# Kernel optimization log

Measured on AMD Instinct MI355X. Metric: run time of the kernel, lower is better.

Reference implementation:

```python
import jax, jax.numpy as jnp
import numpy as np

HEADS = 4
DIM_HEAD = 128


def setup_inputs() -> dict:
    key = jax.random.key(0)
    k1, k2, k3, k4 = jax.random.split(key, 4)
    B, C, H, W = 8, 256, 64, 64
    hidden = HEADS * DIM_HEAD  # 512
    x = jax.random.normal(k1, (B, C, H, W), dtype=jnp.float32)
    # 1x1 convs are just channel matmuls; store kernels as [out_ch, in_ch]
    w_qkv = jax.random.normal(k2, (3 * hidden, C), dtype=jnp.float32) * 0.05
    w_out = jax.random.normal(k3, (C, hidden), dtype=jnp.float32) * 0.05
    b_out = jax.random.normal(k4, (C,), dtype=jnp.float32) * 0.05
    return {"x": x, "w_qkv": w_qkv, "w_out": w_out, "b_out": b_out}


def reference(x, w_qkv, w_out, b_out):
    B, C, H, W = x.shape
    n = H * W
    # to_qkv: 1x1 conv without bias == channel matmul
    qkv = jnp.einsum('bchw,oc->bohw', x, w_qkv)  # [B, 3*heads*dim_head, H, W]
    qkv = qkv.reshape(B, 3, HEADS, DIM_HEAD, n)  # 'b (qkv heads c) h w -> b qkv heads c n'
    q, k, v = qkv[:, 0], qkv[:, 1], qkv[:, 2]    # each [B, heads, dim_head, n]
    k = jax.nn.softmax(k, axis=-1)               # softmax over spatial positions
    context = jnp.einsum('bhdn,bhen->bhde', k, v)   # [B, heads, d, e]
    out = jnp.einsum('bhde,bhdn->bhen', context, q)  # [B, heads, e, n]
    out = out.reshape(B, HEADS * DIM_HEAD, H, W)
    # to_out: 1x1 conv with bias
    return jnp.einsum('bchw,oc->bohw', out, w_out) + b_out[None, :, None, None]
```

## Files before the change

kernel.cpp:

```cpp
#include <hip/hip_runtime.h>
#include <stdint.h>


#define TILE 64
#define BK 16

using frag8 = __attribute__((ext_vector_type(8))) short;
using f32x4 = __attribute__((ext_vector_type(4))) float;

__device__ __forceinline__ float bf2f(unsigned short u) {
    union { unsigned int u; float f; } c;
    c.u = ((unsigned int)u) << 16;
    return c.f;
}
__device__ __forceinline__ unsigned short f2bf(float f) {
    union { float f; unsigned int u; } c; c.f = f;
    unsigned int u = c.u;
    return (unsigned short)((u + 0x7FFFu + ((u >> 16) & 1u)) >> 16);
}

__device__ __forceinline__ void gl_lds16(const void* g, void* l) {
    __builtin_amdgcn_global_load_lds(
        (const __attribute__((address_space(1))) unsigned int*)g,
        (__attribute__((address_space(3))) unsigned int*)l, 16, 0, 0);
}

__global__ __launch_bounds__(256) void k0_wconv(
    const float* __restrict__ w_qkv, unsigned short* __restrict__ wkvb)
{
    const int idx = (blockIdx.x * 256 + threadIdx.x) * 4;
    float4 v = *(const float4*)(w_qkv + 512 * 256 + idx);
    ushort4 o;
    o.x = f2bf(v.x); o.y = f2bf(v.y); o.z = f2bf(v.z); o.w = f2bf(v.w);
    *(ushort4*)(wkvb + idx) = o;
}

__global__ __launch_bounds__(256) void k0_xt(
    const float* __restrict__ x, unsigned short* __restrict__ xbT)
{
    __shared__ float T[64][65];
    const int tid = threadIdx.x;
    const int n0 = blockIdx.x * 64, c0 = blockIdx.y * 64, b = blockIdx.z;
    const float* xb = x + (size_t)b * 1048576;
    const int cr = tid >> 4, nc = (tid & 15) * 4;
    #pragma unroll
    for (int p = 0; p < 4; ++p) {
        float4 v = *(const float4*)(xb + (size_t)(c0 + cr + p * 16) * 4096 + n0 + nc);
        T[cr + p * 16][nc + 0] = v.x; T[cr + p * 16][nc + 1] = v.y;
        T[cr + p * 16][nc + 2] = v.z; T[cr + p * 16][nc + 3] = v.w;
    }
    __syncthreads();
    const int n = tid >> 2, cc = (tid & 3) * 16;
    unsigned short* dst = xbT + (size_t)b * 1048576 + (size_t)(n0 + n) * 256 + c0 + cc;
    #pragma unroll
    for (int g = 0; g < 4; ++g) {
        ushort4 o;
        o.x = f2bf(T[cc + g * 4 + 0][n]);
        o.y = f2bf(T[cc + g * 4 + 1][n]);
        o.z = f2bf(T[cc + g * 4 + 2][n]);
        o.w = f2bf(T[cc + g * 4 + 3][n]);
        *(ushort4*)(dst + g * 4) = o;
    }
}

template<int MODE>
__global__ __launch_bounds__(256) void mfma_bt(
    const unsigned short* __restrict__ A0, int lda,
    const unsigned short* __restrict__ B0, int ldb,
    void* __restrict__ C0, int ldc,
    const float* __restrict__ bias, int Kp,
    unsigned long long sAz, unsigned long long sBz, unsigned long long sCz)
{
    __shared__ unsigned short As[128 * 32];
    __shared__ unsigned short Bs[128 * 32];
    const int tid  = threadIdx.x;
    const int w    = tid >> 6, lane = tid & 63;
    const int quad = lane >> 4, l16 = lane & 15;
    const int wm = (w >> 1) * 64, wn = (w & 1) * 64;
    const int z = blockIdx.z;

    const unsigned short* A;
    const unsigned short* B;
    int ks, ke, m0, n0;
    if constexpr (MODE == 2) {
        m0 = 0; n0 = 0;
        ks = blockIdx.x * 512; ke = ks + 512;
        const unsigned long long off =
            ((unsigned long long)(z >> 2) * 1024ull + (unsigned long long)(z & 3) * 128ull) * 4096ull;
        A = A0 + off; B = B0 + off;
    } else {
        m0 = blockIdx.y * 128; n0 = blockIdx.x * 128;
        ks = 0; ke = Kp;
        A = A0 + sAz * z + (unsigned long long)m0 * lda;
        B = B0 + sBz * z + (unsigned long long)n0 * ldb;
    }

    const int cA0 = w * 128 + lane;
    const int cA1 = cA0 + 64;
    const unsigned short* gA0 = A + (unsigned long long)(cA0 >> 2) * lda + (cA0 & 3) * 8;
    const unsigned short* gA1 = A + (unsigned long long)(cA1 >> 2) * lda + (cA1 & 3) * 8;
    const unsigned short* gB0 = B + (unsigned long long)(cA0 >> 2) * ldb + (cA0 & 3) * 8;
    const unsigned short* gB1 = B + (unsigned long long)(cA1 >> 2) * ldb + (cA1 & 3) * 8;
    unsigned short* lA0 = As + w * 1024;
    unsigned short* lA1 = As + w * 1024 + 512;
    unsigned short* lB0 = Bs + w * 1024;
    unsigned short* lB1 = Bs + w * 1024 + 512;

    f32x4 acc[4][4] = {};

    for (int k0 = ks; k0 < ke; k0 += 32) {
        gl_lds16(gA0 + k0, lA0);
        gl_lds16(gA1 + k0, lA1);
        gl_lds16(gB0 + k0, lB0);
        gl_lds16(gB1 + k0, lB1);
        __syncthreads();
        frag8 a[4], b[4];
        #pragma unroll
        for (int t = 0; t < 4; ++t) {
            a[t] = *(const frag8*)(As + (wm + t * 16 + l16) * 32 + quad * 8);
            b[t] = *(const frag8*)(Bs + (wn + t * 16 + l16) * 32 + quad * 8);
        }
        #pragma unroll
        for (int mt = 0; mt < 4; ++mt)
            #pragma unroll
            for (int nt = 0; nt < 4; ++nt)
                acc[mt][nt] = __builtin_amdgcn_mfma_f32_16x16x32_bf16(
                    a[mt], b[nt], acc[mt][nt], 0, 0, 0);
        __syncthreads();
    }

    if constexpr (MODE == 0) {
        unsigned short* C = (unsigned short*)C0 + sCz * z
                          + (unsigned long long)m0 * ldc + n0;
        #pragma unroll
        for (int mt = 0; mt < 4; ++mt) {
            const int row = wm + mt * 16 + quad * 4;
            #pragma unroll
            for (int nt = 0; nt < 4; ++nt) {
                const int col = wn + nt * 16 + l16;
                #pragma unroll
                for (int r = 0; r < 4; ++r)
                    C[(unsigned long long)(row + r) * ldc + col] = f2bf(acc[mt][nt][r]);
            }
        }
    } else if constexpr (MODE == 1) {
        float* C = (float*)C0 + sCz * z + (unsigned long long)m0 * ldc + n0;
        const float* bp = bias + m0;
        #pragma unroll
        for (int mt = 0; mt < 4; ++mt) {
            const int row = wm + mt * 16 + quad * 4;
            #pragma unroll
            for (int nt = 0; nt < 4; ++nt) {
                const int col = wn + nt * 16 + l16;
                #pragma unroll
                for (int r = 0; r < 4; ++r)
                    C[(unsigned long long)(row + r) * ldc + col] = acc[mt][nt][r] + bp[row + r];
            }
        }
    } else {
        float* C = (float*)C0 + ((unsigned long long)blockIdx.x * 32 + z) * 16384ull;
        #pragma unroll
        for (int mt = 0; mt < 4; ++mt) {
            const int row = wm + mt * 16 + quad * 4;
            #pragma unroll
            for (int nt = 0; nt < 4; ++nt) {
                const int col = wn + nt * 16 + l16;
                #pragma unroll
                for (int r = 0; r < 4; ++r)
                    C[(row + r) * 128 + col] = acc[mt][nt][r];
            }
        }
    }
}

__global__ __launch_bounds__(256) void k2_softmax(unsigned short* __restrict__ kv)
{
    __shared__ float red[4];
    const int idx = blockIdx.x;
    const int b = idx >> 9, r = idx & 511;
    unsigned short* row = kv + (size_t)(b * 1024 + r) * 4096;
    const int tid = threadIdx.x;
    float v[16];
    #pragma unroll
    for (int g = 0; g < 4; ++g) {
        ushort4 u = *(const ushort4*)(row + g * 1024 + tid * 4);
        v[g * 4 + 0] = bf2f(u.x); v[g * 4 + 1] = bf2f(u.y);
        v[g * 4 + 2] = bf2f(u.z); v[g * 4 + 3] = bf2f(u.w);
    }
    float m = -1e30f;
    #pragma unroll
    for (int i = 0; i < 16; ++i) m = fmaxf(m, v[i]);
    #pragma unroll
    for (int off = 32; off > 0; off >>= 1) m = fmaxf(m, __shfl_down(m, off, 64));
    if ((tid & 63) == 0) red[tid >> 6] = m;
    __syncthreads();
    m = fmaxf(fmaxf(red[0], red[1]), fmaxf(red[2], red[3]));
    __syncthreads();
    float s = 0.f;
    #pragma unroll
    for (int i = 0; i < 16; ++i) { v[i] = __expf(v[i] - m); s += v[i]; }
    #pragma unroll
    for (int off = 32; off > 0; off >>= 1) s += __shfl_down(s, off, 64);
    if ((tid & 63) == 0) red[tid >> 6] = s;
    __syncthreads();
    s = red[0] + red[1] + red[2] + red[3];
    const float inv = 1.0f / s;
    #pragma unroll
    for (int g = 0; g < 4; ++g) {
        ushort4 u;
        u.x = f2bf(v[g * 4 + 0] * inv); u.y = f2bf(v[g * 4 + 1] * inv);
        u.z = f2bf(v[g * 4 + 2] * inv); u.w = f2bf(v[g * 4 + 3] * inv);
        *(ushort4*)(row + g * 1024 + tid * 4) = u;
    }
}

__global__ __launch_bounds__(256) void k4_m(
    const float* __restrict__ w_out,
    const float* __restrict__ ctxp, float* __restrict__ M)
{
    __shared__ float As[BK][TILE + 1];
    __shared__ float Bs[BK][TILE + 1];
    const int tid = threadIdx.x;
    const int d0 = blockIdx.x * TILE;
    const int o0 = blockIdx.y * TILE;
    const int bh = blockIdx.z;
    const int bB = bh >> 2, h = bh & 3;
    const int tm = tid >> 4, tn = tid & 15;
    const int lr = tid >> 2, lc = (tid & 3) << 2;
    float acc[4][4] = {};
    for (int e0 = 0; e0 < 128; e0 += BK) {
        float4 a4 = *(const float4*)(w_out + (o0 + lr) * 512 + h * 128 + e0 + lc);
        float4 bsum = make_float4(0.f, 0.f, 0.f, 0.f);
        #pragma unroll
        for (int sl = 0; sl < 8; ++sl) {
            float4 t = *(const float4*)(ctxp + ((size_t)(sl * 32 + bh) * 128 + d0 + lr) * 128 + e0 + lc);
            bsum.x += t.x; bsum.y += t.y; bsum.z += t.z; bsum.w += t.w;
        }
        As[lc + 0][lr] = a4.x; As[lc + 1][lr] = a4.y;
        As[lc + 2][lr] = a4.z; As[lc + 3][lr] = a4.w;
        Bs[lc + 0][lr] = bsum.x; Bs[lc + 1][lr] = bsum.y;
        Bs[lc + 2][lr] = bsum.z; Bs[lc + 3][lr] = bsum.w;
        __syncthreads();
        #pragma unroll
        for (int kk = 0; kk < BK; ++kk) {
            float a[4], bb[4];
            #pragma unroll
            for (int i = 0; i < 4; ++i) a[i] = As[kk][tm * 4 + i];
            #pragma unroll
            for (int j = 0; j < 4; ++j) bb[j] = Bs[kk][tn * 4 + j];
            #pragma unroll
            for (int i = 0; i < 4; ++i)
                #pragma unroll
                for (int j = 0; j < 4; ++j) acc[i][j] += a[i] * bb[j];
        }
        __syncthreads();
    }
    #pragma unroll
    for (int i = 0; i < 4; ++i) {
        float4 o; o.x = acc[i][0]; o.y = acc[i][1]; o.z = acc[i][2]; o.w = acc[i][3];
        *(float4*)(M + (size_t)(bB * 256 + o0 + tm * 4 + i) * 512 + h * 128 + d0 + tn * 4) = o;
    }
}

__global__ __launch_bounds__(256) void k5_n(
    const float* __restrict__ M, const float* __restrict__ w_qkv,
    unsigned short* __restrict__ Nb)
{
    __shared__ float As[BK][TILE + 1];
    __shared__ float Bs[BK][TILE + 1];
    const int tid = threadIdx.x;
    const int c0 = blockIdx.x * TILE;
    const int o0 = blockIdx.y * TILE;
    const int b  = blockIdx.z;
    const int tm = tid >> 4, tn = tid & 15;
    const int lr = tid >> 2, lc = (tid & 3) << 2;
    const int br = tid >> 4, bc = (tid & 15) << 2;
    float acc[4][4] = {};
    for (int j0 = 0; j0 < 512; j0 += BK) {
        float4 a4 = *(const float4*)(M + (size_t)(b * 256 + o0 + lr) * 512 + j0 + lc);
        float4 b4 = *(const float4*)(w_qkv + (size_t)(j0 + br) * 256 + c0 + bc);
        As[lc + 0][lr] = a4.x; As[lc + 1][lr] = a4.y;
        As[lc + 2][lr] = a4.z; As[lc + 3][lr] = a4.w;
        Bs[br][bc + 0] = b4.x; Bs[br][bc + 1] = b4.y;
        Bs[br][bc + 2] = b4.z; Bs[br][bc + 3] = b4.w;
        __syncthreads();
        #pragma unroll
        for (int kk = 0; kk < BK; ++kk) {
            float a[4], bb[4];
            #pragma unroll
            for (int i = 0; i < 4; ++i) a[i] = As[kk][tm * 4 + i];
            #pragma unroll
            for (int j = 0; j < 4; ++j) bb[j] = Bs[kk][tn * 4 + j];
            #pragma unroll
            for (int i = 0; i < 4; ++i)
                #pragma unroll
                for (int j = 0; j < 4; ++j) acc[i][j] += a[i] * bb[j];
        }
        __syncthreads();
    }
    #pragma unroll
    for (int i = 0; i < 4; ++i) {
        ushort4 o4;
        o4.x = f2bf(acc[i][0]); o4.y = f2bf(acc[i][1]);
        o4.z = f2bf(acc[i][2]); o4.w = f2bf(acc[i][3]);
        *(ushort4*)(Nb + (size_t)(b * 256 + o0 + tm * 4 + i) * 256 + c0 + tn * 4) = o4;
    }
}

extern "C" void kernel_launch(void* const* d_in, const int* in_sizes, int n_in,
                              void* d_out, int out_size, void* d_ws, size_t ws_size,
                              hipStream_t stream) {
    (void)in_sizes; (void)n_in; (void)out_size; (void)ws_size;
    const float* x     = (const float*)d_in[0];
    const float* w_qkv = (const float*)d_in[1];
    const float* w_out = (const float*)d_in[2];
    const float* b_out = (const float*)d_in[3];
    float* out = (float*)d_out;

    char* ws = (char*)d_ws;
    unsigned short* kv   = (unsigned short*)ws;
    unsigned short* xbT  = (unsigned short*)(ws + 67108864);
    unsigned short* wkvb = (unsigned short*)(ws + 83886080);
    float*          ctxp = (float*)(ws + 84410368);
    float*          M    = (float*)(ws + 101187584);
    unsigned short* Nb   = (unsigned short*)(ws + 105381888);

    k0_wconv<<<dim3(256), 256, 0, stream>>>(w_qkv, wkvb);
    k0_xt<<<dim3(64, 4, 8), 256, 0, stream>>>(x, xbT);
    mfma_bt<0><<<dim3(32, 8, 8), 256, 0, stream>>>(
        wkvb, 256, xbT, 256, kv, 4096, nullptr, 256,
        0ull, 1048576ull, 4194304ull);
    k2_softmax<<<dim3(4096), 256, 0, stream>>>(kv);
    mfma_bt<2><<<dim3(8, 1, 32), 256, 0, stream>>>(
        kv, 4096, kv + (size_t)512 * 4096, 4096, ctxp, 128, nullptr, 0,
        0ull, 0ull, 0ull);
    k4_m<<<dim3(2, 4, 32), 256, 0, stream>>>(w_out, ctxp, M);
    k5_n<<<dim3(4, 4, 8), 256, 0, stream>>>(M, w_qkv, Nb);
    mfma_bt<1><<<dim3(32, 2, 8), 256, 0, stream>>>(
        Nb, 256, xbT, 256, out, 4096, b_out, 256,
        65536ull, 1048576ull, 1048576ull);
}
```

Measured before the change: 223.5 us.

## Move folded weight-context products onto bf16 MFMA with split-sum prepass

Replaces the two fp32 SIMT tiled GEMMs that built M = W_out·context and N = M·W_q with a small split-K reduction kernel plus two bf16 MFMA GEMM launches, adding a new indexing mode to the shared MFMA kernel. The weight conversion kernel now also converts W_out to bf16 and writes a transposed bf16 copy of W_q. This targets the scalar FMA cost of the small GEMMs, in exchange for more bf16 rounding of intermediates and one extra launch.

```diff
diff --git a/kernel.cpp b/kernel.cpp
--- a/kernel.cpp
+++ b/kernel.cpp
@@ -1,9 +1,6 @@
 #include <hip/hip_runtime.h>
 #include <stdint.h>
 
-
-#define TILE 64
-#define BK 16
 
 using frag8 = __attribute__((ext_vector_type(8))) short;
 using f32x4 = __attribute__((ext_vector_type(4))) float;
@@ -25,14 +22,48 @@
         (__attribute__((address_space(3))) unsigned int*)l, 16, 0, 0);
 }
 
-__global__ __launch_bounds__(256) void k0_wconv(
-    const float* __restrict__ w_qkv, unsigned short* __restrict__ wkvb)
-{
-    const int idx = (blockIdx.x * 256 + threadIdx.x) * 4;
-    float4 v = *(const float4*)(w_qkv + 512 * 256 + idx);
-    ushort4 o;
-    o.x = f2bf(v.x); o.y = f2bf(v.y); o.z = f2bf(v.z); o.w = f2bf(v.w);
-    *(ushort4*)(wkvb + idx) = o;
+__global__ __launch_bounds__(256) void k0_weights(
+    const float* __restrict__ w_qkv, const float* __restrict__ w_out,
+    unsigned short* __restrict__ wkvb, unsigned short* __restrict__ woutb,
+    unsigned short* __restrict__ wqT)
+{
+    __shared__ float T[64][65];
+    const int blk = blockIdx.x;
+    const int tid = threadIdx.x;
+    if (blk < 256) {
+        const int idx = (blk * 256 + tid) * 4;
+        float4 v = *(const float4*)(w_qkv + 512 * 256 + idx);
+        ushort4 o;
+        o.x = f2bf(v.x); o.y = f2bf(v.y); o.z = f2bf(v.z); o.w = f2bf(v.w);
+        *(ushort4*)(wkvb + idx) = o;
+    } else if (blk < 384) {
+        const int idx = ((blk - 256) * 256 + tid) * 4;
+        float4 v = *(const float4*)(w_out + idx);
+        ushort4 o;
+        o.x = f2bf(v.x); o.y = f2bf(v.y); o.z = f2bf(v.z); o.w = f2bf(v.w);
+        *(ushort4*)(woutb + idx) = o;
+    } else {
+        const int t = blk - 384;
+        const int j0 = (t >> 2) * 64, c0 = (t & 3) * 64;
+        const int r = tid >> 4, cc = (tid & 15) * 4;
+        #pragma unroll
+        for (int p = 0; p < 4; ++p) {
+            float4 v = *(const float4*)(w_qkv + (j0 + r + p * 16) * 256 + c0 + cc);
+            T[r + p * 16][cc + 0] = v.x; T[r + p * 16][cc + 1] = v.y;
+            T[r + p * 16][cc + 2] = v.z; T[r + p * 16][cc + 3] = v.w;
+        }
+        __syncthreads();
+        const int c = tid >> 2, jj = (tid & 3) * 16;
+        #pragma unroll
+        for (int g = 0; g < 4; ++g) {
+            ushort4 o;
+            o.x = f2bf(T[jj + g * 4 + 0][c]);
+            o.y = f2bf(T[jj + g * 4 + 1][c]);
+            o.z = f2bf(T[jj + g * 4 + 2][c]);
+            o.w = f2bf(T[jj + g * 4 + 3][c]);
+            *(ushort4*)(wqT + (c0 + c) * 512 + j0 + jj + g * 4) = o;
+        }
+    }
 }
 
 __global__ __launch_bounds__(256) void k0_xt(
@@ -88,6 +119,11 @@
         const unsigned long long off =
             ((unsigned long long)(z >> 2) * 1024ull + (unsigned long long)(z & 3) * 128ull) * 4096ull;
         A = A0 + off; B = B0 + off;
+    } else if constexpr (MODE == 3) {
+        m0 = blockIdx.y * 128; n0 = 0;
+        ks = 0; ke = Kp;
+        A = A0 + (unsigned long long)(z & 3) * 128ull + (unsigned long long)m0 * lda;
+        B = B0 + (unsigned long long)z * 16384ull;
     } else {
         m0 = blockIdx.y * 128; n0 = blockIdx.x * 128;
         ks = 0; ke = Kp;
@@ -129,9 +165,13 @@
         __syncthreads();
     }
 
-    if constexpr (MODE == 0) {
-        unsigned short* C = (unsigned short*)C0 + sCz * z
-                          + (unsigned long long)m0 * ldc + n0;
+    if constexpr (MODE == 0 || MODE == 3) {
+        unsigned short* C;
+        if constexpr (MODE == 0)
+            C = (unsigned short*)C0 + sCz * z + (unsigned long long)m0 * ldc + n0;
+        else
+            C = (unsigned short*)C0 + (unsigned long long)(z >> 2) * 131072ull
+              + (unsigned long long)(z & 3) * 128ull + (unsigned long long)m0 * ldc;
         #pragma unroll
         for (int mt = 0; mt < 4; ++mt) {
             const int row = wm + mt * 16 + quad * 4;
@@ -214,97 +254,19 @@
     }
 }
 
-__global__ __launch_bounds__(256) void k4_m(
-    const float* __restrict__ w_out,
-    const float* __restrict__ ctxp, float* __restrict__ M)
-{
-    __shared__ float As[BK][TILE + 1];
-    __shared__ float Bs[BK][TILE + 1];
-    const int tid = threadIdx.x;
-    const int d0 = blockIdx.x * TILE;
-    const int o0 = blockIdx.y * TILE;
-    const int bh = blockIdx.z;
-    const int bB = bh >> 2, h = bh & 3;
-    const int tm = tid >> 4, tn = tid & 15;
-    const int lr = tid >> 2, lc = (tid & 3) << 2;
-    float acc[4][4] = {};
-    for (int e0 = 0; e0 < 128; e0 += BK) {
-        float4 a4 = *(const float4*)(w_out + (o0 + lr) * 512 + h * 128 + e0 + lc);
-        float4 bsum = make_float4(0.f, 0.f, 0.f, 0.f);
-        #pragma unroll
-        for (int sl = 0; sl < 8; ++sl) {
-            float4 t = *(const float4*)(ctxp + ((size_t)(sl * 32 + bh) * 128 + d0 + lr) * 128 + e0 + lc);
-            bsum.x += t.x; bsum.y += t.y; bsum.z += t.z; bsum.w += t.w;
-        }
-        As[lc + 0][lr] = a4.x; As[lc + 1][lr] = a4.y;
-        As[lc + 2][lr] = a4.z; As[lc + 3][lr] = a4.w;
-        Bs[lc + 0][lr] = bsum.x; Bs[lc + 1][lr] = bsum.y;
-        Bs[lc + 2][lr] = bsum.z; Bs[lc + 3][lr] = bsum.w;
-        __syncthreads();
-        #pragma unroll
-        for (int kk = 0; kk < BK; ++kk) {
-            float a[4], bb[4];
-            #pragma unroll
-            for (int i = 0; i < 4; ++i) a[i] = As[kk][tm * 4 + i];
-            #pragma unroll
-            for (int j = 0; j < 4; ++j) bb[j] = Bs[kk][tn * 4 + j];
-            #pragma unroll
-            for (int i = 0; i < 4; ++i)
-                #pragma unroll
-                for (int j = 0; j < 4; ++j) acc[i][j] += a[i] * bb[j];
-        }
-        __syncthreads();
-    }
-    #pragma unroll
-    for (int i = 0; i < 4; ++i) {
-        float4 o; o.x = acc[i][0]; o.y = acc[i][1]; o.z = acc[i][2]; o.w = acc[i][3];
-        *(float4*)(M + (size_t)(bB * 256 + o0 + tm * 4 + i) * 512 + h * 128 + d0 + tn * 4) = o;
-    }
-}
-
-__global__ __launch_bounds__(256) void k5_n(
-    const float* __restrict__ M, const float* __restrict__ w_qkv,
-    unsigned short* __restrict__ Nb)
-{
-    __shared__ float As[BK][TILE + 1];
-    __shared__ float Bs[BK][TILE + 1];
-    const int tid = threadIdx.x;
-    const int c0 = blockIdx.x * TILE;
-    const int o0 = blockIdx.y * TILE;
-    const int b  = blockIdx.z;
-    const int tm = tid >> 4, tn = tid & 15;
-    const int lr = tid >> 2, lc = (tid & 3) << 2;
-    const int br = tid >> 4, bc = (tid & 15) << 2;
-    float acc[4][4] = {};
-    for (int j0 = 0; j0 < 512; j0 += BK) {
-        float4 a4 = *(const float4*)(M + (size_t)(b * 256 + o0 + lr) * 512 + j0 + lc);
-        float4 b4 = *(const float4*)(w_qkv + (size_t)(j0 + br) * 256 + c0 + bc);
-        As[lc + 0][lr] = a4.x; As[lc + 1][lr] = a4.y;
-        As[lc + 2][lr] = a4.z; As[lc + 3][lr] = a4.w;
-        Bs[br][bc + 0] = b4.x; Bs[br][bc + 1] = b4.y;
-        Bs[br][bc + 2] = b4.z; Bs[br][bc + 3] = b4.w;
-        __syncthreads();
-        #pragma unroll
-        for (int kk = 0; kk < BK; ++kk) {
-            float a[4], bb[4];
-            #pragma unroll
-            for (int i = 0; i < 4; ++i) a[i] = As[kk][tm * 4 + i];
-            #pragma unroll
-            for (int j = 0; j < 4; ++j) bb[j] = Bs[kk][tn * 4 + j];
-            #pragma unroll
-            for (int i = 0; i < 4; ++i)
-                #pragma unroll
-                for (int j = 0; j < 4; ++j) acc[i][j] += a[i] * bb[j];
-        }
-        __syncthreads();
-    }
-    #pragma unroll
-    for (int i = 0; i < 4; ++i) {
-        ushort4 o4;
-        o4.x = f2bf(acc[i][0]); o4.y = f2bf(acc[i][1]);
-        o4.z = f2bf(acc[i][2]); o4.w = f2bf(acc[i][3]);
-        *(ushort4*)(Nb + (size_t)(b * 256 + o0 + tm * 4 + i) * 256 + c0 + tn * 4) = o4;
-    }
+__global__ __launch_bounds__(256) void k3_sum(
+    const float* __restrict__ ctxp, unsigned short* __restrict__ ctxb)
+{
+    const int idx = (blockIdx.x * 256 + threadIdx.x) * 4;
+    float4 s = make_float4(0.f, 0.f, 0.f, 0.f);
+    #pragma unroll
+    for (int sl = 0; sl < 8; ++sl) {
+        float4 t = *(const float4*)(ctxp + (size_t)sl * 524288 + idx);
+        s.x += t.x; s.y += t.y; s.z += t.z; s.w += t.w;
+    }
+    ushort4 o;
+    o.x = f2bf(s.x); o.y = f2bf(s.y); o.z = f2bf(s.z); o.w = f2bf(s.w);
+    *(ushort4*)(ctxb + idx) = o;
 }
 
 extern "C" void kernel_launch(void* const* d_in, const int* in_sizes, int n_in,
@@ -318,14 +280,17 @@
     float* out = (float*)d_out;
 
     char* ws = (char*)d_ws;
-    unsigned short* kv   = (unsigned short*)ws;
-    unsigned short* xbT  = (unsigned short*)(ws + 67108864);
-    unsigned short* wkvb = (unsigned short*)(ws + 83886080);
-    float*          ctxp = (float*)(ws + 84410368);
-    float*          M    = (float*)(ws + 101187584);
-    unsigned short* Nb   = (unsigned short*)(ws + 105381888);
-
-    k0_wconv<<<dim3(256), 256, 0, stream>>>(w_qkv, wkvb);
+    unsigned short* kv    = (unsigned short*)ws;
+    unsigned short* xbT   = (unsigned short*)(ws + 67108864);
+    unsigned short* wkvb  = (unsigned short*)(ws + 83886080);
+    unsigned short* woutb = (unsigned short*)(ws + 84410368);
+    unsigned short* wqT   = (unsigned short*)(ws + 84672512);
+    float*          ctxp  = (float*)(ws + 84934656);
+    unsigned short* ctxb  = (unsigned short*)(ws + 101711872);
+    unsigned short* Mb    = (unsigned short*)(ws + 102760448);
+    unsigned short* Nb    = (unsigned short*)(ws + 104857600);
+
+    k0_weights<<<dim3(416), 256, 0, stream>>>(w_qkv, w_out, wkvb, woutb, wqT);
     k0_xt<<<dim3(64, 4, 8), 256, 0, stream>>>(x, xbT);
     mfma_bt<0><<<dim3(32, 8, 8), 256, 0, stream>>>(
         wkvb, 256, xbT, 256, kv, 4096, nullptr, 256,
@@ -334,8 +299,13 @@
     mfma_bt<2><<<dim3(8, 1, 32), 256, 0, stream>>>(
         kv, 4096, kv + (size_t)512 * 4096, 4096, ctxp, 128, nullptr, 0,
         0ull, 0ull, 0ull);
-    k4_m<<<dim3(2, 4, 32), 256, 0, stream>>>(w_out, ctxp, M);
-    k5_n<<<dim3(4, 4, 8), 256, 0, stream>>>(M, w_qkv, Nb);
+    k3_sum<<<dim3(512), 256, 0, stream>>>(ctxp, ctxb);
+    mfma_bt<3><<<dim3(1, 2, 32), 256, 0, stream>>>(
+        woutb, 512, ctxb, 128, Mb, 512, nullptr, 128,
+        0ull, 0ull, 0ull);
+    mfma_bt<0><<<dim3(2, 2, 8), 256, 0, stream>>>(
+        Mb, 512, wqT, 512, Nb, 256, nullptr, 512,
+        131072ull, 0ull, 65536ull);
     mfma_bt<1><<<dim3(32, 2, 8), 256, 0, stream>>>(
         Nb, 256, xbT, 256, out, 4096, b_out, 256,
         65536ull, 1048576ull, 1048576ull);
```

New measurement: 184.5 us. 17.4% less time.
